# Kernel tuning notes

Hardware: AMD Instinct MI355X
Metric: run time of the kernel (lower is better)

Reference implementation:

```python
import jax, jax.numpy as jnp
import numpy as np

B, N_TOK, D = 32, 1024, 1024
CH, PS, NP = 3, 16, 32  # channels, patch_size, n_patches (sample_size // patch_size)
EPS = 1e-5


def setup_inputs() -> dict:
    key = jax.random.key(0)
    k1, k2 = jax.random.split(key)
    x = jax.random.normal(k1, (B, N_TOK, D), dtype=jnp.float32)
    ln_w = jnp.ones((D,), dtype=jnp.float32)
    ln_b = jnp.zeros((D,), dtype=jnp.float32)
    W = jax.random.normal(k2, (CH * PS * PS, D), dtype=jnp.float32) * (1.0 / np.sqrt(D))
    b = jnp.zeros((CH * PS * PS,), dtype=jnp.float32)
    return {"x": x, "ln_w": ln_w, "ln_b": ln_b, "W": W, "b": b}


def reference(x, ln_w, ln_b, W, b):
    # LayerNorm over last dim
    mean = jnp.mean(x, axis=-1, keepdims=True)
    var = jnp.mean(jnp.square(x - mean), axis=-1, keepdims=True)
    h = (x - mean) * jax.lax.rsqrt(var + EPS) * ln_w + ln_b
    # SiLU
    h = h * jax.nn.sigmoid(h)
    # Linear: [B, N, D] @ [D, ph*pw*c] + bias
    y = jnp.einsum('bnd,od->bno', h, W) + b  # [B, N_TOK, PS*PS*CH]
    # rearrange 'b (h w) (ph pw c) -> b c (h ph) (w pw)'
    y = y.reshape(B, NP, NP, PS, PS, CH)           # b h w ph pw c
    y = y.transpose(0, 5, 1, 3, 2, 4)              # b c h ph w pw
    y = y.reshape(B, CH, NP * PS, NP * PS)
    return y
```

## Files before the change

kernel.cpp:

```cpp
#include <hip/hip_runtime.h>
#include <hip/hip_bf16.h>

#define M_TOT 32768
#define DDIM  1024
#define ODIM  768
#define LN_EPS 1e-5f

typedef __attribute__((__ext_vector_type__(8))) short bf16x8;
typedef __attribute__((__ext_vector_type__(4))) float f32x4;

__device__ __forceinline__ unsigned short f2bf(float f) {
  union { __hip_bfloat16 h; unsigned short u; } cv;
  cv.h = __float2bfloat16(f);
  return cv.u;
}

__device__ __forceinline__ float silu_f(float v) {
  return v / (1.f + __expf(-v));
}

__global__ void wconv_kernel(const float4* __restrict__ Wf, ushort4* __restrict__ Wb, int n4) {
  int i = blockIdx.x * blockDim.x + threadIdx.x;
  if (i >= n4) return;
  float4 v = Wf[i];
  ushort4 o;
  o.x = f2bf(v.x); o.y = f2bf(v.y); o.z = f2bf(v.z); o.w = f2bf(v.w);
  Wb[i] = o;
}

__global__ __launch_bounds__(256)
void ln_silu_kernel(const float* __restrict__ x, const float* __restrict__ lnw,
                    const float* __restrict__ lnb, __hip_bfloat16* __restrict__ h)
{
  const int tid  = threadIdx.x;
  const int lane = tid & 63;
  const int wid  = tid >> 6;
  const int row  = blockIdx.x * 4 + wid;

  const float4* xr = (const float4*)(x + (size_t)row * DDIM);
  float4 v[4];
#pragma unroll
  for (int jj = 0; jj < 4; ++jj) v[jj] = xr[lane + 64 * jj];

  float s = 0.f, ss = 0.f;
#pragma unroll
  for (int jj = 0; jj < 4; ++jj) {
    float4 a = v[jj];
    s  += a.x + a.y + a.z + a.w;
    ss += a.x * a.x + a.y * a.y + a.z * a.z + a.w * a.w;
  }
#pragma unroll
  for (int off = 1; off < 64; off <<= 1) {
    s  += __shfl_xor(s, off);
    ss += __shfl_xor(ss, off);
  }
  const float mean = s * (1.f / 1024.f);
  const float rstd = rsqrtf(ss * (1.f / 1024.f) - mean * mean + LN_EPS);

  ushort4* hr = (ushort4*)(h + (size_t)row * DDIM);
#pragma unroll
  for (int jj = 0; jj < 4; ++jj) {
    float4 wv = ((const float4*)lnw)[lane + 64 * jj];
    float4 bv = ((const float4*)lnb)[lane + 64 * jj];
    float4 a  = v[jj];
    float e0 = silu_f((a.x - mean) * rstd * wv.x + bv.x);
    float e1 = silu_f((a.y - mean) * rstd * wv.y + bv.y);
    float e2 = silu_f((a.z - mean) * rstd * wv.z + bv.z);
    float e3 = silu_f((a.w - mean) * rstd * wv.w + bv.w);
    ushort4 o; o.x = f2bf(e0); o.y = f2bf(e1); o.z = f2bf(e2); o.w = f2bf(e3);
    hr[lane + 64 * jj] = o;
  }
}

#define GBM 256
#define GBN 192
#define ABY 16384
#define BUFB 28672
#define VMW(n) asm volatile("s_waitcnt vmcnt(" #n ")" ::: "memory")

__device__ __forceinline__ void gload16(const void* g, void* l) {
  __builtin_amdgcn_global_load_lds(
      (const __attribute__((address_space(1))) unsigned int*)g,
      (__attribute__((address_space(3))) unsigned int*)l, 16, 0, 0);
}

__global__ __launch_bounds__(512, 2)
void gemm_kernel(const __hip_bfloat16* __restrict__ h,
                 const __hip_bfloat16* __restrict__ Wb,
                 const float* __restrict__ bias,
                 float* __restrict__ out)
{
  __shared__ char smem[3 * BUFB];
  const int tid  = threadIdx.x;
  const int lane = tid & 63;
  const int w    = tid >> 6;

  const int wg = blockIdx.x;
  const int sv = ((wg & 7) << 6) + (wg >> 3);
  const int mt = sv >> 2, nt = sv & 3;
  const int m0 = mt << 8, n0 = nt * GBN;

  const int aR0 = tid >> 2;
  const __hip_bfloat16* aP0 = h + (size_t)(m0 + aR0) * DDIM + (((tid & 3) ^ (aR0 & 3)) << 3);
  const int s1  = 512 + tid;
  const int aR1 = s1 >> 2;
  const __hip_bfloat16* aP1 = h + (size_t)(m0 + aR1) * DDIM + (((s1 & 3) ^ (aR1 & 3)) << 3);
  const int bR0 = tid >> 2;
  const __hip_bfloat16* bP0 = Wb + (size_t)(n0 + bR0) * DDIM + (((tid & 3) ^ (bR0 & 3)) << 3);
  const int bR1 = s1 >> 2;
  const __hip_bfloat16* bP1 = Wb + (size_t)(n0 + bR1) * DDIM + (((s1 & 3) ^ (bR1 & 3)) << 3);
  const bool half = (tid < 256);

  const int wm = w >> 1, wn = w & 1;
  const int lr = lane & 15, lq = lane >> 4;
  int aRd[4], bRd[6];
#pragma unroll
  for (int i = 0; i < 4; ++i) {
    int row = wm * 64 + i * 16 + lr;
    aRd[i] = row * 64 + ((lq ^ (row & 3)) << 4);
  }
#pragma unroll
  for (int j = 0; j < 6; ++j) {
    int row = wn * 96 + j * 16 + lr;
    bRd[j] = ABY + row * 64 + ((lq ^ (row & 3)) << 4);
  }

  auto stP0 = [&](int t) {
    const int k0 = t << 5;
    char* b = smem + (t % 3) * BUFB;
    gload16(aP0 + k0, b + (tid << 4));
    gload16(bP0 + k0, b + ABY + (tid << 4));
  };
  auto stP1 = [&](int t) {
    const int k0 = t << 5;
    char* b = smem + (t % 3) * BUFB;
    gload16(aP1 + k0, b + (s1 << 4));
    if (half) gload16(bP1 + k0, b + ABY + (s1 << 4));
  };

  f32x4 acc[4][6];
#pragma unroll
  for (int i = 0; i < 4; ++i)
#pragma unroll
    for (int j = 0; j < 6; ++j)
      acc[i][j] = (f32x4){0.f, 0.f, 0.f, 0.f};

  stP0(0); stP1(0); stP0(1); stP1(1);

  for (int t = 0; t < 32; ++t) {
    if (t < 31) { if (half) VMW(4); else VMW(3); }
    else        { VMW(0); }
    __builtin_amdgcn_s_barrier();
    asm volatile("" ::: "memory");

    const char* bb = smem + (t % 3) * BUFB;
    if (t < 30) stP0(t + 2);
    bf16x8 af[4], bf0[3];
#pragma unroll
    for (int i = 0; i < 4; ++i) af[i]  = *(const bf16x8*)(bb + aRd[i]);
#pragma unroll
    for (int j = 0; j < 3; ++j) bf0[j] = *(const bf16x8*)(bb + bRd[j]);
    __builtin_amdgcn_s_setprio(1);
#pragma unroll
    for (int i = 0; i < 4; ++i)
#pragma unroll
      for (int j = 0; j < 3; ++j)
        acc[i][j] = __builtin_amdgcn_mfma_f32_16x16x32_bf16(af[i], bf0[j], acc[i][j], 0, 0, 0);
    __builtin_amdgcn_s_setprio(0);
    asm volatile("" ::: "memory");
    __builtin_amdgcn_s_barrier();
    asm volatile("" ::: "memory");
    if (t < 30) stP1(t + 2);
    bf16x8 bf1[3];
#pragma unroll
    for (int j = 0; j < 3; ++j) bf1[j] = *(const bf16x8*)(bb + bRd[3 + j]);
    __builtin_amdgcn_s_setprio(1);
#pragma unroll
    for (int i = 0; i < 4; ++i)
#pragma unroll
      for (int j = 0; j < 3; ++j)
        acc[i][3 + j] = __builtin_amdgcn_mfma_f32_16x16x32_bf16(af[i], bf1[j], acc[i][3 + j], 0, 0, 0);
    __builtin_amdgcn_s_setprio(0);
  }

  const int b   = m0 >> 10;
  const int hq0 = (m0 & 1023) >> 5;
  float bv[6]; int cj[6], pwj[6], prj[6];
#pragma unroll
  for (int j = 0; j < 6; ++j) {
    int o = wn * 96 + j * 16 + lr;
    bv[j]  = bias[n0 + o];
    cj[j]  = o % 3;
    int oq = o / 3;
    pwj[j] = oq & 15;
    prj[j] = o / 48;
  }
  float* ldsF = (float*)smem;

#pragma unroll
  for (int g = 0; g < 16; ++g) {
    if (wm == (g >> 2)) {
      const int i_f = g & 3;
#pragma unroll
      for (int j = 0; j < 6; ++j)
#pragma unroll
        for (int r = 0; r < 4; ++r) {
          const int tk = lq * 4 + r;
          ldsF[((cj[j] * 4 + prj[j]) << 8) + ((tk ^ (cj[j] & 1)) << 4) + (pwj[j] ^ (lq << 2))] =
              acc[i_f][j][r] + bv[j];
        }
    }
    __syncthreads();
    const int hh = hq0 + (g >> 1);
#pragma unroll
    for (int q = 0; q < 2; ++q) {
      if (q == 1 && tid >= 256) break;
      const int f   = (q << 9) + tid;
      const int c   = f >> 8;
      const int pr  = (f >> 6) & 3;
      const int tk  = (f >> 2) & 15;
      const int pw0 = (f & 3) << 2;
      const int lqw = tk >> 2;
      float4 v = *(const float4*)(ldsF + (((c * 4 + pr) << 8) + ((tk ^ (c & 1)) << 4)
                                          + (pw0 ^ (lqw << 2))));
      const size_t idx = (((size_t)(b * 3 + c)) << 18)
                       + (size_t)((hh << 4) + (nt << 2) + pr) * 512
                       + ((g & 1) << 8) + (tk << 4) + pw0;
      *(float4*)(out + idx) = v;
    }
    __syncthreads();
  }
}

#define BM 64
#define BK 32
#define NTHR 1024
#define LDS_BYTES 53760

__global__ __launch_bounds__(NTHR, 4)
void fused_kernel(const float* __restrict__ x,
                  const float* __restrict__ lnw,
                  const float* __restrict__ lnb,
                  const float* __restrict__ Wf,
                  const float* __restrict__ bias,
                  float* __restrict__ out)
{
  extern __shared__ char smem[];
  char* AsBase = smem;
  char* BsBase = smem + 4096;
  float* smean = (float*)(smem + 53248);
  float* srstd = smean + BM;

  const int tid = threadIdx.x;
  const int m0  = blockIdx.x * BM;
  const int bb   = m0 >> 10;
  const int h0   = (m0 & 1023) >> 5;

  {
    const int row = tid >> 4;
    const int sub = tid & 15;
    const float4* xr = (const float4*)(x + (size_t)(m0 + row) * DDIM);
    float s = 0.f, ss = 0.f;
#pragma unroll 4
    for (int j = 0; j < 16; ++j) {
      float4 v = xr[sub + (j << 4)];
      s  += v.x + v.y + v.z + v.w;
      ss += v.x * v.x + v.y * v.y + v.z * v.z + v.w * v.w;
    }
#pragma unroll
    for (int off = 1; off < 16; off <<= 1) {
      s  += __shfl_xor(s, off);
      ss += __shfl_xor(ss, off);
    }
    if (sub == 0) {
      float mean = s * (1.f / 1024.f);
      float var  = ss * (1.f / 1024.f) - mean * mean;
      smean[row] = mean;
      srstd[row] = rsqrtf(var + LN_EPS);
    }
  }
  __syncthreads();

  const int arow  = tid >> 4;
  const int acol2 = tid & 15;
  const int aOff  = (m0 + arow) * DDIM + (acol2 << 1);
  const int aDst  = (arow << 6) + ((((acol2 >> 2) ^ ((arow >> 2) & 3)) << 4)) + ((acol2 & 3) << 2);
  const float aMean = smean[arow];
  const float aRstd = srstd[arow];

  int bOffF[6], bDstF[6];
#pragma unroll
  for (int c = 0; c < 6; ++c) {
    int idx = tid + (c << 10);
    int r = idx >> 3, c4 = idx & 7;
    bOffF[c] = r * DDIM + (c4 << 2);
    bDstF[c] = (r << 6) + ((((c4 >> 1) ^ ((r >> 2) & 3)) << 4)) + ((c4 & 1) << 3);
  }

  const int lane = tid & 63;
  const int wid  = tid >> 6;
  const int lr   = lane & 15;
  const int lq   = lane >> 4;
  const int kswz = (lq ^ ((lr >> 2) & 3)) << 4;
  int aRd[4], bRd[3];
#pragma unroll
  for (int i = 0; i < 4; ++i) aRd[i] = (((i << 4) + lr) << 6) + kswz;
#pragma unroll
  for (int j = 0; j < 3; ++j) bRd[j] = ((wid * 48 + (j << 4) + lr) << 6) + kswz;

  float2 aReg, lwReg, lbReg;
  float4 bRegF[6];

  auto loadTile = [&](int tt) {
    const int k0 = tt * BK;
    aReg  = *(const float2*)(x + aOff + k0);
    lwReg = *(const float2*)(lnw + (acol2 << 1) + k0);
    lbReg = *(const float2*)(lnb + (acol2 << 1) + k0);
#pragma unroll
    for (int c = 0; c < 6; ++c)
      bRegF[c] = *(const float4*)(Wf + bOffF[c] + k0);
  };

  auto storeTile = [&]() {
    float hx = (aReg.x - aMean) * aRstd * lwReg.x + lbReg.x;
    float hy = (aReg.y - aMean) * aRstd * lwReg.y + lbReg.y;
    hx = silu_f(hx); hy = silu_f(hy);
    ushort2 ap; ap.x = f2bf(hx); ap.y = f2bf(hy);
    *(ushort2*)(AsBase + aDst) = ap;
#pragma unroll
    for (int c = 0; c < 6; ++c) {
      float4 wv = bRegF[c];
      ushort4 bp; bp.x = f2bf(wv.x); bp.y = f2bf(wv.y); bp.z = f2bf(wv.z); bp.w = f2bf(wv.w);
      *(ushort4*)(BsBase + bDstF[c]) = bp;
    }
  };

  f32x4 acc[4][3];
#pragma unroll
  for (int i = 0; i < 4; ++i)
#pragma unroll
    for (int j = 0; j < 3; ++j)
      acc[i][j] = (f32x4){0.f, 0.f, 0.f, 0.f};

  loadTile(0);
  storeTile();
  __syncthreads();

  for (int t = 0; t < 32; ++t) {
    if (t < 31) loadTile(t + 1);
    bf16x8 af[4], bfr[3];
#pragma unroll
    for (int i = 0; i < 4; ++i) af[i] = *(const bf16x8*)(AsBase + aRd[i]);
#pragma unroll
    for (int j = 0; j < 3; ++j) bfr[j] = *(const bf16x8*)(BsBase + bRd[j]);
#pragma unroll
    for (int i = 0; i < 4; ++i)
#pragma unroll
      for (int j = 0; j < 3; ++j)
        acc[i][j] = __builtin_amdgcn_mfma_f32_16x16x32_bf16(af[i], bfr[j], acc[i][j], 0, 0, 0);
    __syncthreads();
    if (t < 31) storeTile();
    __syncthreads();
  }

  float* ldsF = (float*)smem;
  float bv[3]; int cv[3], phv[3], pwv[3];
#pragma unroll
  for (int j = 0; j < 3; ++j) {
    const int o = wid * 48 + (j << 4) + lr;
    bv[j]  = bias[o];
    cv[j]  = o % 3;
    const int oq = o / 3;
    pwv[j] = oq & 15;
    phv[j] = oq >> 4;
  }

#pragma unroll
  for (int i = 0; i < 4; ++i) {
#pragma unroll
    for (int j = 0; j < 3; ++j) {
#pragma unroll
      for (int r = 0; r < 4; ++r) {
        const int wl  = (lq << 2) + r;
        const int lin = ((cv[j] * 16 + phv[j]) << 8) + (wl << 4) + pwv[j];
        const int dws = lin ^ (cv[j] << 2) ^ (((lin >> 6) & 1) << 4);
        ldsF[dws] = acc[i][j][r] + bv[j];
      }
    }
    __syncthreads();
    const int hq = h0 + (i >> 1);
    const int w0 = (i & 1) << 4;
#pragma unroll
    for (int q = 0; q < 3; ++q) {
      const int g4  = (q << 10) + tid;
      const int dw  = g4 << 2;
      const int run = dw >> 8;
      const int c   = run >> 4;
      const int ph  = run & 15;
      const int wl  = (dw >> 4) & 15;
      const int pw  = dw & 15;
      const int dws = dw ^ (c << 2) ^ (((dw >> 6) & 1) << 4);
      float4 v = *(const float4*)(ldsF + dws);
      const size_t idx = (((size_t)(bb * 3 + c)) << 18)
                       + ((size_t)((hq << 4) + ph) << 9)
                       + ((w0 + wl) << 4) + pw;
      *(float4*)(out + idx) = v;
    }
    __syncthreads();
  }
}

extern "C" void kernel_launch(void* const* d_in, const int* in_sizes, int n_in,
                              void* d_out, int out_size, void* d_ws, size_t ws_size,
                              hipStream_t stream) {
  const float* x    = (const float*)d_in[0];
  const float* lnw  = (const float*)d_in[1];
  const float* lnb  = (const float*)d_in[2];
  const float* W    = (const float*)d_in[3];
  const float* bias = (const float*)d_in[4];
  float* out = (float*)d_out;

  const size_t wbBytes = (size_t)ODIM * DDIM * sizeof(__hip_bfloat16);
  const size_t hBytes  = (size_t)M_TOT * DDIM * sizeof(__hip_bfloat16);
  __hip_bfloat16* Wb = (__hip_bfloat16*)d_ws;
  __hip_bfloat16* hb = (__hip_bfloat16*)((char*)d_ws + wbBytes);

  if (ws_size >= wbBytes + hBytes) {
    wconv_kernel<<<dim3(768), dim3(256), 0, stream>>>((const float4*)W, (ushort4*)Wb,
                                                      ODIM * DDIM / 4);
    ln_silu_kernel<<<dim3(M_TOT / 4), dim3(256), 0, stream>>>(x, lnw, lnb, hb);
    gemm_kernel<<<dim3((M_TOT / GBM) * (ODIM / GBN)), dim3(512), 0, stream>>>(hb, Wb, bias, out);
  } else {
    fused_kernel<<<dim3(M_TOT / BM), dim3(NTHR), LDS_BYTES, stream>>>(
        x, lnw, lnb, W, bias, out);
  }
}
```

Baseline: 109.8 us.

## Fuse LayerNorm+SiLU into GEMM A-tile staging, drop bf16 activation buffer

Replaces the separate LayerNorm/SiLU pass and the GEMM with one kernel. Each block owns 64 rows and the full 768 output columns. It computes row statistics up front, then streams x, normalizes and applies SiLU, converts to bf16 and writes into LDS while bf16 W tiles arrive through global_load_lds into a double buffer. This removes the round trip of the 64 MB bf16 intermediate through HBM. In exchange, x is read twice (once for stats, once for the GEMM), the full W is re-streamed by every block, and LDS use is large (~115 KB), which limits occupancy.

```diff
diff --git a/kernel.cpp b/kernel.cpp
--- a/kernel.cpp
+++ b/kernel.cpp
@@ -28,114 +28,114 @@
   Wb[i] = o;
 }
 
-__global__ __launch_bounds__(256)
-void ln_silu_kernel(const float* __restrict__ x, const float* __restrict__ lnw,
-                    const float* __restrict__ lnb, __hip_bfloat16* __restrict__ h)
-{
-  const int tid  = threadIdx.x;
-  const int lane = tid & 63;
-  const int wid  = tid >> 6;
-  const int row  = blockIdx.x * 4 + wid;
-
-  const float4* xr = (const float4*)(x + (size_t)row * DDIM);
-  float4 v[4];
-#pragma unroll
-  for (int jj = 0; jj < 4; ++jj) v[jj] = xr[lane + 64 * jj];
-
-  float s = 0.f, ss = 0.f;
-#pragma unroll
-  for (int jj = 0; jj < 4; ++jj) {
-    float4 a = v[jj];
-    s  += a.x + a.y + a.z + a.w;
-    ss += a.x * a.x + a.y * a.y + a.z * a.z + a.w * a.w;
-  }
-#pragma unroll
-  for (int off = 1; off < 64; off <<= 1) {
-    s  += __shfl_xor(s, off);
-    ss += __shfl_xor(ss, off);
-  }
-  const float mean = s * (1.f / 1024.f);
-  const float rstd = rsqrtf(ss * (1.f / 1024.f) - mean * mean + LN_EPS);
-
-  ushort4* hr = (ushort4*)(h + (size_t)row * DDIM);
-#pragma unroll
-  for (int jj = 0; jj < 4; ++jj) {
-    float4 wv = ((const float4*)lnw)[lane + 64 * jj];
-    float4 bv = ((const float4*)lnb)[lane + 64 * jj];
-    float4 a  = v[jj];
-    float e0 = silu_f((a.x - mean) * rstd * wv.x + bv.x);
-    float e1 = silu_f((a.y - mean) * rstd * wv.y + bv.y);
-    float e2 = silu_f((a.z - mean) * rstd * wv.z + bv.z);
-    float e3 = silu_f((a.w - mean) * rstd * wv.w + bv.w);
-    ushort4 o; o.x = f2bf(e0); o.y = f2bf(e1); o.z = f2bf(e2); o.w = f2bf(e3);
-    hr[lane + 64 * jj] = o;
-  }
-}
-
-#define GBM 256
-#define GBN 192
-#define ABY 16384
-#define BUFB 28672
-#define VMW(n) asm volatile("s_waitcnt vmcnt(" #n ")" ::: "memory")
-
 __device__ __forceinline__ void gload16(const void* g, void* l) {
   __builtin_amdgcn_global_load_lds(
       (const __attribute__((address_space(1))) unsigned int*)g,
       (__attribute__((address_space(3))) unsigned int*)l, 16, 0, 0);
 }
 
+#define VMW(n) asm volatile("s_waitcnt vmcnt(" #n ")" ::: "memory")
+
+#define FBUF 53248
+#define FABY 4096
+#define LNW_OFF 106496
+#define LNB_OFF 110592
+#define STAT_OFF 114688
+
 __global__ __launch_bounds__(512, 2)
-void gemm_kernel(const __hip_bfloat16* __restrict__ h,
-                 const __hip_bfloat16* __restrict__ Wb,
-                 const float* __restrict__ bias,
-                 float* __restrict__ out)
+void fusedln_gemm_kernel(const float* __restrict__ x,
+                         const float* __restrict__ lnw,
+                         const float* __restrict__ lnb,
+                         const __hip_bfloat16* __restrict__ Wb,
+                         const float* __restrict__ bias,
+                         float* __restrict__ out)
 {
-  __shared__ char smem[3 * BUFB];
+  __shared__ char smem[115200];
   const int tid  = threadIdx.x;
   const int lane = tid & 63;
   const int w    = tid >> 6;
-
-  const int wg = blockIdx.x;
-  const int sv = ((wg & 7) << 6) + (wg >> 3);
-  const int mt = sv >> 2, nt = sv & 3;
-  const int m0 = mt << 8, n0 = nt * GBN;
-
-  const int aR0 = tid >> 2;
-  const __hip_bfloat16* aP0 = h + (size_t)(m0 + aR0) * DDIM + (((tid & 3) ^ (aR0 & 3)) << 3);
-  const int s1  = 512 + tid;
-  const int aR1 = s1 >> 2;
-  const __hip_bfloat16* aP1 = h + (size_t)(m0 + aR1) * DDIM + (((s1 & 3) ^ (aR1 & 3)) << 3);
-  const int bR0 = tid >> 2;
-  const __hip_bfloat16* bP0 = Wb + (size_t)(n0 + bR0) * DDIM + (((tid & 3) ^ (bR0 & 3)) << 3);
-  const int bR1 = s1 >> 2;
-  const __hip_bfloat16* bP1 = Wb + (size_t)(n0 + bR1) * DDIM + (((s1 & 3) ^ (bR1 & 3)) << 3);
-  const bool half = (tid < 256);
-
-  const int wm = w >> 1, wn = w & 1;
+  const int m0   = blockIdx.x << 6;
+
+  float* lnw_s = (float*)(smem + LNW_OFF);
+  float* lnb_s = (float*)(smem + LNB_OFF);
+  float* smean = (float*)(smem + STAT_OFF);
+  float* srstd = smean + 64;
+
+  {
+    lnw_s[tid]       = lnw[tid];
+    lnw_s[tid + 512] = lnw[tid + 512];
+    lnb_s[tid]       = lnb[tid];
+    lnb_s[tid + 512] = lnb[tid + 512];
+    const int row = tid >> 3;
+    const int sub = tid & 7;
+    const float4* xr = (const float4*)(x + (size_t)(m0 + row) * DDIM);
+    float s = 0.f, ss = 0.f;
+#pragma unroll 8
+    for (int j = 0; j < 32; ++j) {
+      float4 v = xr[sub + (j << 3)];
+      s  += v.x + v.y + v.z + v.w;
+      ss += v.x * v.x + v.y * v.y + v.z * v.z + v.w * v.w;
+    }
+#pragma unroll
+    for (int off = 1; off < 8; off <<= 1) {
+      s  += __shfl_xor(s, off);
+      ss += __shfl_xor(ss, off);
+    }
+    if (sub == 0) {
+      float mean = s * (1.f / 1024.f);
+      float var  = ss * (1.f / 1024.f) - mean * mean;
+      smean[row] = mean;
+      srstd[row] = rsqrtf(var + LN_EPS);
+    }
+  }
+  __syncthreads();
+
+  const int arow = tid >> 3;
+  const int ak4  = tid & 7;
+  const float aMean = smean[arow];
+  const float aRstd = srstd[arow];
+  const float* aSrc = x + (size_t)(m0 + arow) * DDIM + (ak4 << 2);
+  const int aDst = (arow << 6) + ((((ak4 >> 1) ^ (arow & 3)) << 4)) + ((ak4 & 1) << 3);
+
+  const __hip_bfloat16* bP[6];
+  int bDst[6];
+#pragma unroll
+  for (int q = 0; q < 6; ++q) {
+    int s   = (q << 9) + tid;
+    int row = s >> 2, chk = s & 3;
+    bP[q]   = Wb + (size_t)row * DDIM + ((chk ^ (row & 3)) << 3);
+    bDst[q] = FABY + (s << 4);
+  }
+
   const int lr = lane & 15, lq = lane >> 4;
   int aRd[4], bRd[6];
 #pragma unroll
   for (int i = 0; i < 4; ++i) {
-    int row = wm * 64 + i * 16 + lr;
+    int row = i * 16 + lr;
     aRd[i] = row * 64 + ((lq ^ (row & 3)) << 4);
   }
 #pragma unroll
   for (int j = 0; j < 6; ++j) {
-    int row = wn * 96 + j * 16 + lr;
-    bRd[j] = ABY + row * 64 + ((lq ^ (row & 3)) << 4);
-  }
-
-  auto stP0 = [&](int t) {
+    int row = w * 96 + j * 16 + lr;
+    bRd[j] = FABY + row * 64 + ((lq ^ (row & 3)) << 4);
+  }
+
+  auto stageB = [&](int t) {
+    char* b = smem + (t & 1) * FBUF;
     const int k0 = t << 5;
-    char* b = smem + (t % 3) * BUFB;
-    gload16(aP0 + k0, b + (tid << 4));
-    gload16(bP0 + k0, b + ABY + (tid << 4));
+#pragma unroll
+    for (int q = 0; q < 6; ++q) gload16(bP[q] + k0, b + bDst[q]);
   };
-  auto stP1 = [&](int t) {
-    const int k0 = t << 5;
-    char* b = smem + (t % 3) * BUFB;
-    gload16(aP1 + k0, b + (s1 << 4));
-    if (half) gload16(bP1 + k0, b + ABY + (s1 << 4));
+  auto putA = [&](int t, float4 ax) {
+    const int k = (t << 5) + (ak4 << 2);
+    float4 wv = *(const float4*)(lnw_s + k);
+    float4 bv = *(const float4*)(lnb_s + k);
+    float h0 = silu_f((ax.x - aMean) * aRstd * wv.x + bv.x);
+    float h1 = silu_f((ax.y - aMean) * aRstd * wv.y + bv.y);
+    float h2 = silu_f((ax.z - aMean) * aRstd * wv.z + bv.z);
+    float h3 = silu_f((ax.w - aMean) * aRstd * wv.w + bv.w);
+    ushort4 o; o.x = f2bf(h0); o.y = f2bf(h1); o.z = f2bf(h2); o.w = f2bf(h3);
+    *(ushort4*)(smem + (t & 1) * FBUF + aDst) = o;
   };
 
   f32x4 acc[4][6];
@@ -145,87 +145,91 @@
     for (int j = 0; j < 6; ++j)
       acc[i][j] = (f32x4){0.f, 0.f, 0.f, 0.f};
 
-  stP0(0); stP1(0); stP0(1); stP1(1);
-
-  for (int t = 0; t < 32; ++t) {
-    if (t < 31) { if (half) VMW(4); else VMW(3); }
-    else        { VMW(0); }
+  {
+    float4 ax0 = *(const float4*)(aSrc);
+    stageB(0);
+    VMW(6);
+    putA(0, ax0);
+    asm volatile("s_waitcnt lgkmcnt(0)" ::: "memory");
     __builtin_amdgcn_s_barrier();
     asm volatile("" ::: "memory");
-
-    const char* bb = smem + (t % 3) * BUFB;
-    if (t < 30) stP0(t + 2);
-    bf16x8 af[4], bf0[3];
+  }
+
+  for (int t = 0; t < 32; ++t) {
+    float4 axn;
+    if (t < 31) {
+      axn = *(const float4*)(aSrc + ((t + 1) << 5));
+      stageB(t + 1);
+    }
+    if (t < 31) VMW(7); else VMW(0);
+    __builtin_amdgcn_sched_barrier(0);
+
+    const char* bb = smem + (t & 1) * FBUF;
+    bf16x8 af[4], bfq[6];
 #pragma unroll
     for (int i = 0; i < 4; ++i) af[i]  = *(const bf16x8*)(bb + aRd[i]);
 #pragma unroll
-    for (int j = 0; j < 3; ++j) bf0[j] = *(const bf16x8*)(bb + bRd[j]);
+    for (int j = 0; j < 6; ++j) bfq[j] = *(const bf16x8*)(bb + bRd[j]);
+
     __builtin_amdgcn_s_setprio(1);
 #pragma unroll
     for (int i = 0; i < 4; ++i)
 #pragma unroll
-      for (int j = 0; j < 3; ++j)
-        acc[i][j] = __builtin_amdgcn_mfma_f32_16x16x32_bf16(af[i], bf0[j], acc[i][j], 0, 0, 0);
+      for (int j = 0; j < 6; ++j)
+        acc[i][j] = __builtin_amdgcn_mfma_f32_16x16x32_bf16(af[i], bfq[j], acc[i][j], 0, 0, 0);
     __builtin_amdgcn_s_setprio(0);
-    asm volatile("" ::: "memory");
+
+    if (t < 31) {
+      VMW(6);
+      putA(t + 1, axn);
+    }
+    asm volatile("s_waitcnt lgkmcnt(0)" ::: "memory");
     __builtin_amdgcn_s_barrier();
     asm volatile("" ::: "memory");
-    if (t < 30) stP1(t + 2);
-    bf16x8 bf1[3];
-#pragma unroll
-    for (int j = 0; j < 3; ++j) bf1[j] = *(const bf16x8*)(bb + bRd[3 + j]);
-    __builtin_amdgcn_s_setprio(1);
-#pragma unroll
-    for (int i = 0; i < 4; ++i)
-#pragma unroll
-      for (int j = 0; j < 3; ++j)
-        acc[i][3 + j] = __builtin_amdgcn_mfma_f32_16x16x32_bf16(af[i], bf1[j], acc[i][3 + j], 0, 0, 0);
-    __builtin_amdgcn_s_setprio(0);
   }
 
   const int b   = m0 >> 10;
   const int hq0 = (m0 & 1023) >> 5;
-  float bv[6]; int cj[6], pwj[6], prj[6];
+  float bv[6]; int cj[6], pwj[6], phj[6];
 #pragma unroll
   for (int j = 0; j < 6; ++j) {
-    int o = wn * 96 + j * 16 + lr;
-    bv[j]  = bias[n0 + o];
+    int o = w * 96 + j * 16 + lr;
+    bv[j]  = bias[o];
     cj[j]  = o % 3;
     int oq = o / 3;
     pwj[j] = oq & 15;
-    prj[j] = o / 48;
+    phj[j] = oq >> 4;
   }
   float* ldsF = (float*)smem;
 
 #pragma unroll
-  for (int g = 0; g < 16; ++g) {
-    if (wm == (g >> 2)) {
-      const int i_f = g & 3;
+  for (int g = 0; g < 2; ++g) {
+#pragma unroll
+    for (int ii = 0; ii < 2; ++ii) {
+      const int i = (g << 1) | ii;
 #pragma unroll
       for (int j = 0; j < 6; ++j)
 #pragma unroll
         for (int r = 0; r < 4; ++r) {
-          const int tk = lq * 4 + r;
-          ldsF[((cj[j] * 4 + prj[j]) << 8) + ((tk ^ (cj[j] & 1)) << 4) + (pwj[j] ^ (lq << 2))] =
-              acc[i_f][j][r] + bv[j];
+          const int tk = (ii << 4) | (lq << 2) | r;
+          const int f  = (((cj[j] << 4) | phj[j]) << 9) | (tk << 4) | (pwj[j] ^ (lq << 2));
+          ldsF[f] = acc[i][j][r] + bv[j];
         }
     }
     __syncthreads();
-    const int hh = hq0 + (g >> 1);
-#pragma unroll
-    for (int q = 0; q < 2; ++q) {
-      if (q == 1 && tid >= 256) break;
-      const int f   = (q << 9) + tid;
-      const int c   = f >> 8;
-      const int pr  = (f >> 6) & 3;
-      const int tk  = (f >> 2) & 15;
-      const int pw0 = (f & 3) << 2;
-      const int lqw = tk >> 2;
-      float4 v = *(const float4*)(ldsF + (((c * 4 + pr) << 8) + ((tk ^ (c & 1)) << 4)
-                                          + (pw0 ^ (lqw << 2))));
+    const int hh = hq0 + g;
+#pragma unroll
+    for (int u = 0; u < 12; ++u) {
+      const int fl  = ((u << 9) + tid) << 2;
+      const int c   = fl >> 13;
+      const int ph  = (fl >> 9) & 15;
+      const int tk  = (fl >> 4) & 31;
+      const int pw0 = fl & 12;
+      const int lqw = (tk >> 2) & 3;
+      float4 v = *(const float4*)(ldsF + ((fl & ~15) | (pw0 ^ (lqw << 2))));
       const size_t idx = (((size_t)(b * 3 + c)) << 18)
-                       + (size_t)((hh << 4) + (nt << 2) + pr) * 512
-                       + ((g & 1) << 8) + (tk << 4) + pw0;
+                       + (size_t)((hh << 4) + ph) * 512
+                       + (tk << 4) + pw0;
       *(float4*)(out + idx) = v;
     }
     __syncthreads();
@@ -421,15 +425,13 @@
   float* out = (float*)d_out;
 
   const size_t wbBytes = (size_t)ODIM * DDIM * sizeof(__hip_bfloat16);
-  const size_t hBytes  = (size_t)M_TOT * DDIM * sizeof(__hip_bfloat16);
   __hip_bfloat16* Wb = (__hip_bfloat16*)d_ws;
-  __hip_bfloat16* hb = (__hip_bfloat16*)((char*)d_ws + wbBytes);
-
-  if (ws_size >= wbBytes + hBytes) {
+
+  if (ws_size >= wbBytes) {
     wconv_kernel<<<dim3(768), dim3(256), 0, stream>>>((const float4*)W, (ushort4*)Wb,
                                                       ODIM * DDIM / 4);
-    ln_silu_kernel<<<dim3(M_TOT / 4), dim3(256), 0, stream>>>(x, lnw, lnb, hb);
-    gemm_kernel<<<dim3((M_TOT / GBM) * (ODIM / GBN)), dim3(512), 0, stream>>>(hb, Wb, bias, out);
+    fusedln_gemm_kernel<<<dim3(M_TOT / 64), dim3(512), 0, stream>>>(
+        x, lnw, lnb, Wb, bias, out);
   } else {
     fused_kernel<<<dim3(M_TOT / BM), dim3(NTHR), LDS_BYTES, stream>>>(
         x, lnw, lnb, W, bias, out);
```

New measurement: 140.0 us. 27.4% more time.

## Deepen GEMM LDS pipeline to four stages and change swizzle pattern

Applied to the files above, without the earlier changes.

The bf16 GEMM moves from a 3-buffer to a 4-buffer LDS ring, prefetching three k-tiles ahead with adjusted vmcnt waits, and regroups the staging so the A and B tiles are issued in separate phases. It adds extra barriers and explicit lgkmcnt waits with sched_barrier around the MFMA phases. The LDS XOR swizzle now keys on (row>>1)&3 instead of row&3, meant to reduce bank conflicts. The epilogue swizzle on the channel bit is dropped. The larger LDS footprint (about 112KB per block) and the extra barriers may reduce occupancy or add stalls.

```diff
diff --git a/kernel.cpp b/kernel.cpp
--- a/kernel.cpp
+++ b/kernel.cpp
@@ -74,15 +74,16 @@
 
 #define GBM 256
 #define GBN 192
-#define ABY 16384
-#define BUFB 28672
-#define VMW(n) asm volatile("s_waitcnt vmcnt(" #n ")" ::: "memory")
+#define ABYTES 16384
+#define BUFB   28672
 
 __device__ __forceinline__ void gload16(const void* g, void* l) {
   __builtin_amdgcn_global_load_lds(
       (const __attribute__((address_space(1))) unsigned int*)g,
       (__attribute__((address_space(3))) unsigned int*)l, 16, 0, 0);
 }
+
+#define VMW(n) asm volatile("s_waitcnt vmcnt(" #n ")" ::: "memory")
 
 __global__ __launch_bounds__(512, 2)
 void gemm_kernel(const __hip_bfloat16* __restrict__ h,
@@ -90,7 +91,7 @@
                  const float* __restrict__ bias,
                  float* __restrict__ out)
 {
-  __shared__ char smem[3 * BUFB];
+  __shared__ char smem[4 * BUFB];
   const int tid  = threadIdx.x;
   const int lane = tid & 63;
   const int w    = tid >> 6;
@@ -100,16 +101,26 @@
   const int mt = sv >> 2, nt = sv & 3;
   const int m0 = mt << 8, n0 = nt * GBN;
 
-  const int aR0 = tid >> 2;
-  const __hip_bfloat16* aP0 = h + (size_t)(m0 + aR0) * DDIM + (((tid & 3) ^ (aR0 & 3)) << 3);
-  const int s1  = 512 + tid;
-  const int aR1 = s1 >> 2;
-  const __hip_bfloat16* aP1 = h + (size_t)(m0 + aR1) * DDIM + (((s1 & 3) ^ (aR1 & 3)) << 3);
-  const int bR0 = tid >> 2;
-  const __hip_bfloat16* bP0 = Wb + (size_t)(n0 + bR0) * DDIM + (((tid & 3) ^ (bR0 & 3)) << 3);
-  const int bR1 = s1 >> 2;
-  const __hip_bfloat16* bP1 = Wb + (size_t)(n0 + bR1) * DDIM + (((s1 & 3) ^ (bR1 & 3)) << 3);
-  const bool half = (tid < 256);
+  const __hip_bfloat16* aP[2]; int aD[2];
+#pragma unroll
+  for (int q = 0; q < 2; ++q) {
+    int s = (q << 9) + tid;
+    int row = s >> 2, chk = s & 3;
+    aP[q] = h + (size_t)(m0 + row) * DDIM + ((chk ^ ((row >> 1) & 3)) << 3);
+    aD[q] = s << 4;
+  }
+  const bool roleB = (tid < 256);
+  const __hip_bfloat16* bP0; int bD0;
+  const __hip_bfloat16* bP1; int bD1;
+  {
+    int s = tid, row = s >> 2, chk = s & 3;
+    bP0 = Wb + (size_t)(n0 + row) * DDIM + ((chk ^ ((row >> 1) & 3)) << 3);
+    bD0 = ABYTES + (s << 4);
+    int s2 = 512 + (tid & 255);
+    int r2 = s2 >> 2, c2 = s2 & 3;
+    bP1 = Wb + (size_t)(n0 + r2) * DDIM + ((c2 ^ ((r2 >> 1) & 3)) << 3);
+    bD1 = ABYTES + (s2 << 4);
+  }
 
   const int wm = w >> 1, wn = w & 1;
   const int lr = lane & 15, lq = lane >> 4;
@@ -117,25 +128,25 @@
 #pragma unroll
   for (int i = 0; i < 4; ++i) {
     int row = wm * 64 + i * 16 + lr;
-    aRd[i] = row * 64 + ((lq ^ (row & 3)) << 4);
+    aRd[i] = row * 64 + ((lq ^ ((row >> 1) & 3)) << 4);
   }
 #pragma unroll
   for (int j = 0; j < 6; ++j) {
     int row = wn * 96 + j * 16 + lr;
-    bRd[j] = ABY + row * 64 + ((lq ^ (row & 3)) << 4);
-  }
-
-  auto stP0 = [&](int t) {
+    bRd[j] = ABYTES + row * 64 + ((lq ^ ((row >> 1) & 3)) << 4);
+  }
+
+  auto stageA = [&](int t) {
+    char* b = smem + (t & 3) * BUFB;
     const int k0 = t << 5;
-    char* b = smem + (t % 3) * BUFB;
-    gload16(aP0 + k0, b + (tid << 4));
-    gload16(bP0 + k0, b + ABY + (tid << 4));
+    gload16(aP[0] + k0, b + aD[0]);
+    gload16(aP[1] + k0, b + aD[1]);
   };
-  auto stP1 = [&](int t) {
+  auto stageB = [&](int t) {
+    char* b = smem + (t & 3) * BUFB;
     const int k0 = t << 5;
-    char* b = smem + (t % 3) * BUFB;
-    gload16(aP1 + k0, b + (s1 << 4));
-    if (half) gload16(bP1 + k0, b + ABY + (s1 << 4));
+    gload16(bP0 + k0, b + bD0);
+    if (roleB) gload16(bP1 + k0, b + bD1);
   };
 
   f32x4 acc[4][6];
@@ -145,21 +156,28 @@
     for (int j = 0; j < 6; ++j)
       acc[i][j] = (f32x4){0.f, 0.f, 0.f, 0.f};
 
-  stP0(0); stP1(0); stP0(1); stP1(1);
+  stageA(0); stageB(0);
+  stageA(1); stageB(1);
+  stageA(2); stageB(2);
 
   for (int t = 0; t < 32; ++t) {
-    if (t < 31) { if (half) VMW(4); else VMW(3); }
-    else        { VMW(0); }
+    if (t <= 29)      { if (roleB) VMW(8); else VMW(6); }
+    else if (t == 30) { if (roleB) VMW(4); else VMW(3); }
+    else              { VMW(0); }
     __builtin_amdgcn_s_barrier();
     asm volatile("" ::: "memory");
 
-    const char* bb = smem + (t % 3) * BUFB;
-    if (t < 30) stP0(t + 2);
-    bf16x8 af[4], bf0[3];
+    const char* bb = smem + (t & 3) * BUFB;
+    bf16x8 af[4], bf0[3], bf1[3];
+
 #pragma unroll
     for (int i = 0; i < 4; ++i) af[i]  = *(const bf16x8*)(bb + aRd[i]);
 #pragma unroll
     for (int j = 0; j < 3; ++j) bf0[j] = *(const bf16x8*)(bb + bRd[j]);
+    if (t < 29) stageA(t + 3);
+    __builtin_amdgcn_s_barrier();
+    asm volatile("s_waitcnt lgkmcnt(0)" ::: "memory");
+    __builtin_amdgcn_sched_barrier(0);
     __builtin_amdgcn_s_setprio(1);
 #pragma unroll
     for (int i = 0; i < 4; ++i)
@@ -169,11 +187,13 @@
     __builtin_amdgcn_s_setprio(0);
     asm volatile("" ::: "memory");
     __builtin_amdgcn_s_barrier();
-    asm volatile("" ::: "memory");
-    if (t < 30) stP1(t + 2);
-    bf16x8 bf1[3];
+
 #pragma unroll
     for (int j = 0; j < 3; ++j) bf1[j] = *(const bf16x8*)(bb + bRd[3 + j]);
+    if (t < 29) stageB(t + 3);
+    __builtin_amdgcn_s_barrier();
+    asm volatile("s_waitcnt lgkmcnt(0)" ::: "memory");
+    __builtin_amdgcn_sched_barrier(0);
     __builtin_amdgcn_s_setprio(1);
 #pragma unroll
     for (int i = 0; i < 4; ++i)
@@ -181,10 +201,12 @@
       for (int j = 0; j < 3; ++j)
         acc[i][3 + j] = __builtin_amdgcn_mfma_f32_16x16x32_bf16(af[i], bf1[j], acc[i][3 + j], 0, 0, 0);
     __builtin_amdgcn_s_setprio(0);
+    asm volatile("" ::: "memory");
+    __builtin_amdgcn_s_barrier();
   }
 
   const int b   = m0 >> 10;
-  const int hq0 = (m0 & 1023) >> 5;
+  const int hl0 = (m0 & 1023) >> 5;
   float bv[6]; int cj[6], pwj[6], prj[6];
 #pragma unroll
   for (int j = 0; j < 6; ++j) {
@@ -193,7 +215,7 @@
     cj[j]  = o % 3;
     int oq = o / 3;
     pwj[j] = oq & 15;
-    prj[j] = o / 48;
+    prj[j] = oq >> 4;
   }
   float* ldsF = (float*)smem;
 
@@ -206,22 +228,22 @@
 #pragma unroll
         for (int r = 0; r < 4; ++r) {
           const int tk = lq * 4 + r;
-          ldsF[((cj[j] * 4 + prj[j]) << 8) + ((tk ^ (cj[j] & 1)) << 4) + (pwj[j] ^ (lq << 2))] =
+          ldsF[((cj[j] * 4 + prj[j]) << 8) + (tk << 4) + (pwj[j] ^ (lq << 2))] =
               acc[i_f][j][r] + bv[j];
         }
     }
     __syncthreads();
-    const int hh = hq0 + (g >> 1);
-#pragma unroll
-    for (int q = 0; q < 2; ++q) {
-      if (q == 1 && tid >= 256) break;
-      const int f   = (q << 9) + tid;
+    const int hh = hl0 + (g >> 1);
+#pragma unroll
+    for (int u = 0; u < 2; ++u) {
+      if (u == 1 && tid >= 256) break;
+      const int f   = (u << 9) + tid;
       const int c   = f >> 8;
       const int pr  = (f >> 6) & 3;
       const int tk  = (f >> 2) & 15;
       const int pw0 = (f & 3) << 2;
       const int lqw = tk >> 2;
-      float4 v = *(const float4*)(ldsF + (((c * 4 + pr) << 8) + ((tk ^ (c & 1)) << 4)
+      float4 v = *(const float4*)(ldsF + (((c * 4 + pr) << 8) + (tk << 4)
                                           + (pw0 ^ (lqw << 2))));
       const size_t idx = (((size_t)(b * 3 + c)) << 18)
                        + (size_t)((hh << 4) + (nt << 2) + pr) * 512
```

Measured after the change: 109.0 us. Within noise of the previous version (-0.7%).
